# Kernel optimization log

Hardware: AMD Instinct MI355X
Metric: run time of the kernel (lower is better)

The kernel has to match this reference:

```python
import jax, jax.numpy as jnp
import numpy as np

HIDDEN = 1024
INTER = 4096
N_EXPERTS = 8


def geglu(x, w1, w2, w3):
    # x: [N, C], w1/w2: [C, I], w3: [I, C]
    return (jax.nn.gelu(x @ w1, approximate=False) * (x @ w2)) @ w3


def setup_inputs() -> dict:
    key = jax.random.key(0)
    ks = jax.random.split(key, 8)
    s = 0.02
    x = jax.random.normal(ks[0], (2, 2048, HIDDEN), dtype=jnp.float32)
    w1s = jax.random.normal(ks[1], (HIDDEN, INTER), dtype=jnp.float32) * s
    w2s = jax.random.normal(ks[2], (HIDDEN, INTER), dtype=jnp.float32) * s
    w3s = jax.random.normal(ks[3], (INTER, HIDDEN), dtype=jnp.float32) * s
    W1 = jax.random.normal(ks[4], (N_EXPERTS, HIDDEN, INTER), dtype=jnp.float32) * s
    W2 = jax.random.normal(ks[5], (N_EXPERTS, HIDDEN, INTER), dtype=jnp.float32) * s
    W3 = jax.random.normal(ks[6], (N_EXPERTS, INTER, HIDDEN), dtype=jnp.float32) * s
    Wg = jax.random.normal(ks[7], (HIDDEN, N_EXPERTS), dtype=jnp.float32) * s
    return {"x": x, "w1s": w1s, "w2s": w2s, "w3s": w3s,
            "W1": W1, "W2": W2, "W3": W3, "Wg": Wg}


def reference(x, w1s, w2s, w3s, W1, W2, W3, Wg):
    B, T, C = x.shape
    xf = x.reshape(-1, C)  # [N, C]
    shared = geglu(xf, w1s, w2s, w3s)  # [N, C]
    logits = xf @ Wg  # [N, E]
    # top-1 of softmax == argmax of logits (softmax is monotone);
    # NOTE: original torch code does NOT multiply by the routing prob.
    idx = jnp.argmax(logits, axis=-1)  # [N]
    final = jnp.zeros_like(xf)
    for e in range(N_EXPERTS):  # small fixed expert count
        y = geglu(xf, W1[e], W2[e], W3[e])  # [N, C]
        final = final + jnp.where((idx == e)[:, None], y, 0.0)
    return (shared + final).reshape(B, T, C)
```

## Files before the change

### kernel.cpp

```cpp
#include <hip/hip_runtime.h>
#include <stdint.h>

#define HIDDEN 1024
#define INTER  4096
#define NTOK   4096
#define HROWS  (2*NTOK)
#define MAXB1  40
#define MAXB2  72
#define NMAT   27

typedef unsigned short u16;
typedef unsigned int   u32;
typedef __bf16  bf16x8 __attribute__((ext_vector_type(8)));
typedef float   f32x4  __attribute__((ext_vector_type(4)));
typedef u32     u32x4  __attribute__((ext_vector_type(4)));

#define WAITVM(N) asm volatile("s_waitcnt vmcnt(" #N ")" ::: "memory")

__device__ __forceinline__ void hard_barrier() {
  asm volatile("" ::: "memory");
  __builtin_amdgcn_s_barrier();
  asm volatile("" ::: "memory");
}

__device__ __forceinline__ u16 f2bf(float f) {
  u32 u = __float_as_uint(f);
  u32 r = u + 0x7FFFu + ((u >> 16) & 1u);
  return (u16)(r >> 16);
}

__device__ __forceinline__ u32 cvt_pk_bf16(float lo, float hi) {
  u32 r;
  asm("v_cvt_pk_bf16_f32 %0, %1, %2" : "=v"(r) : "v"(lo), "v"(hi));
  return r;
}

__device__ __forceinline__ void glds16(const void* g, void* l) {
  __builtin_amdgcn_global_load_lds(
      (const __attribute__((address_space(1))) void*)g,
      (__attribute__((address_space(3))) void*)l, 16, 0, 0);
}


__global__ void k_init(int* cnt, int* fill) {
  if (threadIdx.x < 8) { cnt[threadIdx.x] = 0; fill[threadIdx.x] = 0; }
}

__global__ __launch_bounds__(256) void k_gate(const float* __restrict__ x,
                                              const float* __restrict__ wg,
                                              int* __restrict__ idx,
                                              int* __restrict__ cnt) {
  int wave = threadIdx.x >> 6, lane = threadIdx.x & 63;
  int t = blockIdx.x * 4 + wave;
  if (t >= NTOK) return;
  float acc[8];
  #pragma unroll
  for (int e = 0; e < 8; ++e) acc[e] = 0.f;
  const float* xr = x + (size_t)t * HIDDEN;
  for (int c = lane; c < HIDDEN; c += 64) {
    float xv = xr[c];
    const float* wrow = wg + (size_t)c * 8;
    #pragma unroll
    for (int e = 0; e < 8; ++e) acc[e] += xv * wrow[e];
  }
  #pragma unroll
  for (int e = 0; e < 8; ++e)
    for (int s = 32; s; s >>= 1) acc[e] += __shfl_xor(acc[e], s);
  if (lane == 0) {
    int best = 0; float bv = acc[0];
    #pragma unroll
    for (int e = 1; e < 8; ++e) if (acc[e] > bv) { bv = acc[e]; best = e; }
    idx[t] = best;
    atomicAdd(&cnt[best], 1);
  }
}

__global__ void k_cvt(const float* __restrict__ x, u16* __restrict__ xb, int n4) {
  int i = blockIdx.x * blockDim.x + threadIdx.x;
  if (i >= n4) return;
  float4 v = ((const float4*)x)[i];
  ushort4 o;
  o.x = f2bf(v.x); o.y = f2bf(v.y); o.z = f2bf(v.z); o.w = f2bf(v.w);
  ((ushort4*)xb)[i] = o;
}

__global__ void k_table(const int* __restrict__ cnt, int* __restrict__ off,
                        int4* __restrict__ tab1, int* __restrict__ nblk1,
                        int4* __restrict__ tab2, int* __restrict__ nblk2) {
  if (threadIdx.x != 0 || blockIdx.x != 0) return;
  int o = 0;
  int offs[8];
  for (int e = 0; e < 8; ++e) { offs[e] = o; off[e] = o; o += cnt[e]; }
  int nb = 0;
  for (int m = 0; m < NTOK / 256; ++m)
    tab1[nb++] = make_int4(8, m * 256, 256, 0);
  for (int e = 0; e < 8; ++e)
    for (int j = 0; j * 256 < cnt[e]; ++j) {
      int rows = cnt[e] - j * 256; if (rows > 256) rows = 256;
      tab1[nb++] = make_int4(e, NTOK + offs[e] + j * 256, rows, offs[e] + j * 256);
    }
  *nblk1 = nb;
  nb = 0;
  for (int m = 0; m < NTOK / 128; ++m)
    tab2[nb++] = make_int4(8, m * 128, 128, 0);
  for (int e = 0; e < 8; ++e)
    for (int j = 0; j * 128 < cnt[e]; ++j) {
      int rows = cnt[e] - j * 128; if (rows > 128) rows = 128;
      tab2[nb++] = make_int4(e, NTOK + offs[e] + j * 128, rows, offs[e] + j * 128);
    }
  *nblk2 = nb;
}

__global__ void k_scatter(const int* __restrict__ idx, const int* __restrict__ off,
                          int* __restrict__ fill, int* __restrict__ perm) {
  int t = blockIdx.x * blockDim.x + threadIdx.x;
  if (t >= NTOK) return;
  int e = idx[t];
  int p = atomicAdd(&fill[e], 1);
  perm[off[e] + p] = t;
}


__global__ __launch_bounds__(256) void k_wcvt(
    const float* __restrict__ w1s, const float* __restrict__ w2s,
    const float* __restrict__ w3s, const float* __restrict__ W1,
    const float* __restrict__ W2,  const float* __restrict__ W3,
    u16* __restrict__ Wb)
{
  int bid = blockIdx.x;
  int m = bid >> 9, pair = bid & 511;
  const float* src; int N, nkt, kt, pp2;
  if (m < 18) {
    N = INTER; nkt = 32;
    int mm = (m < 9) ? m : m - 9;
    const float* sp = (m < 9) ? w1s : w2s;
    const float* ep = (m < 9) ? W1 : W2;
    src = (mm == 0) ? sp : ep + (size_t)(mm - 1) * HIDDEN * INTER;
    kt = pair >> 4; pp2 = pair & 15;
  } else {
    N = HIDDEN; nkt = 128;
    int mm = m - 18;
    src = (mm == 0) ? w3s : W3 + (size_t)(mm - 1) * INTER * HIDDEN;
    kt = pair >> 2; pp2 = pair & 3;
  }

  __shared__ float tileF[32 * 256];
  int tid = threadIdx.x;
  const float* in0 = src + (size_t)(kt * 32) * N + pp2 * 256;
  #pragma unroll
  for (int i = 0; i < 8; ++i) {
    int f = tid + 256 * i;
    int k = f >> 6, c4 = f & 63;
    *(float4*)&tileF[k * 256 + c4 * 4] = *(const float4*)(in0 + (size_t)k * N + c4 * 4);
  }
  __syncthreads();

  int p2 = tid >> 7, n = tid & 127;
  int pidx = m * 1024 + (pp2 * 2 + p2) * nkt + kt;
  u16* outp = Wb + (size_t)pidx * 4096 + n * 32;
  #pragma unroll
  for (int s = 0; s < 4; ++s) {
    int k8 = s ^ ((n >> 1) & 3);
    const float* col = &tileF[(k8 * 8) * 256 + p2 * 128 + n];
    u32x4 pk;
    pk.x = cvt_pk_bf16(col[0],    col[256]);
    pk.y = cvt_pk_bf16(col[512],  col[768]);
    pk.z = cvt_pk_bf16(col[1024], col[1280]);
    pk.w = cvt_pk_bf16(col[1536], col[1792]);
    *(u32x4*)(outp + s * 8) = pk;
  }
}


#define MLP1_TILE(B, STG, WN)                                                        \
  do {                                                                               \
    const u16* LA = pAr  + (B) * 16384;                                              \
    const u16* L1 = pBr1 + (B) * 16384;                                              \
    const u16* L2 = pBr2 + (B) * 16384;                                              \
    bf16x8 af[8], f1[2], f2[2];                                                      \
    _Pragma("unroll")                                                                \
    for (int mi = 0; mi < 4; ++mi) af[mi] = *(const bf16x8*)(LA + mi * 512);         \
    _Pragma("unroll")                                                                \
    for (int ni = 0; ni < 2; ++ni) {                                                 \
      f1[ni] = *(const bf16x8*)(L1 + ni * 512);                                      \
      f2[ni] = *(const bf16x8*)(L2 + ni * 512);                                      \
    }                                                                                \
    if (STG) {                                                                       \
      char* Ld = smem + (((B) + 3) & 3) * 32768;                                     \
      glds16(srcA0, Ld + w * 2048);                                                  \
      glds16(srcA1, Ld + w * 2048 + 1024);                                           \
      srcA0 += 64; srcA1 += 64;                                                      \
    }                                                                                \
    __builtin_amdgcn_s_setprio(1);                                                   \
    _Pragma("unroll")                                                                \
    for (int mi = 0; mi < 4; ++mi) {                                                 \
      acc1[mi][0] = __builtin_amdgcn_mfma_f32_16x16x32_bf16(af[mi], f1[0], acc1[mi][0], 0, 0, 0); \
      acc1[mi][1] = __builtin_amdgcn_mfma_f32_16x16x32_bf16(af[mi], f1[1], acc1[mi][1], 0, 0, 0); \
      acc2[mi][0] = __builtin_amdgcn_mfma_f32_16x16x32_bf16(af[mi], f2[0], acc2[mi][0], 0, 0, 0); \
      acc2[mi][1] = __builtin_amdgcn_mfma_f32_16x16x32_bf16(af[mi], f2[1], acc2[mi][1], 0, 0, 0); \
    }                                                                                \
    __builtin_amdgcn_s_setprio(0);                                                   \
    hard_barrier();                                                                  \
    _Pragma("unroll")                                                                \
    for (int mi = 4; mi < 8; ++mi) af[mi] = *(const bf16x8*)(LA + mi * 512);         \
    if (STG) {                                                                       \
      char* Ld = smem + (((B) + 3) & 3) * 32768;                                     \
      glds16(srcB1, Ld + 16384 + w * 1024);                                          \
      glds16(srcB2, Ld + 24576 + w * 1024);                                          \
      srcB1 += 8192; srcB2 += 8192;                                                  \
    }                                                                                \
    __builtin_amdgcn_s_setprio(1);                                                   \
    _Pragma("unroll")                                                                \
    for (int mi = 4; mi < 8; ++mi) {                                                 \
      acc1[mi][0] = __builtin_amdgcn_mfma_f32_16x16x32_bf16(af[mi], f1[0], acc1[mi][0], 0, 0, 0); \
      acc1[mi][1] = __builtin_amdgcn_mfma_f32_16x16x32_bf16(af[mi], f1[1], acc1[mi][1], 0, 0, 0); \
      acc2[mi][0] = __builtin_amdgcn_mfma_f32_16x16x32_bf16(af[mi], f2[0], acc2[mi][0], 0, 0, 0); \
      acc2[mi][1] = __builtin_amdgcn_mfma_f32_16x16x32_bf16(af[mi], f2[1], acc2[mi][1], 0, 0, 0); \
    }                                                                                \
    __builtin_amdgcn_s_setprio(0);                                                   \
    WN;                                                                              \
    hard_barrier();                                                                  \
  } while (0)

__global__ __launch_bounds__(512, 2) void k_mlp1(
    const u16* __restrict__ xb, const u16* __restrict__ Wb,
    const int* __restrict__ perm, const int4* __restrict__ tab,
    const int* __restrict__ nblk, u16* __restrict__ Hbuf)
{
  int bx = blockIdx.x;
  if (bx >= *nblk) return;
  int4 te = tab[bx];
  int g = te.x, hrow0 = te.y, rows = te.z, pb = te.w;
  int m1 = (g == 8) ? 0 : 1 + g;
  int pp = blockIdx.y;
  int nbase = pp * 128;

  extern __shared__ __align__(16) char smem[];
  int tid = threadIdx.x;
  int w = tid >> 6, lane = tid & 63;
  int q = lane >> 4, rl = lane & 15;
  int mw = w >> 2, nw = w & 3;

  int tokj[2];
  #pragma unroll
  for (int j = 0; j < 2; ++j) {
    int r = w * 32 + j * 16 + (lane >> 2);
    int rc = (r < rows) ? r : (rows - 1);
    tokj[j] = (g == 8) ? (hrow0 + rc) : perm[pb + rc];
  }
  int gch = ((lane & 3) ^ ((lane >> 3) & 3)) * 16;

  const char* srcA0 = (const char*)xb + (size_t)tokj[0] * 2048 + gch;
  const char* srcA1 = (const char*)xb + (size_t)tokj[1] * 2048 + gch;
  const char* srcB1 = (const char*)Wb + ((size_t)m1 * 1024 + pp * 32) * 8192 + (tid << 4);
  const char* srcB2 = (const char*)Wb + ((size_t)(m1 + 9) * 1024 + pp * 32) * 8192 + (tid << 4);

  int co = (q ^ ((rl >> 1) & 3)) * 8;
  const u16* pAr  = (const u16*)smem + (mw * 128 + rl) * 32 + co;
  const u16* pBr1 = (const u16*)smem + 8192  + (nw * 32 + rl) * 32 + co;
  const u16* pBr2 = (const u16*)smem + 12288 + (nw * 32 + rl) * 32 + co;

  f32x4 acc1[8][2], acc2[8][2];
  f32x4 z = {0.f, 0.f, 0.f, 0.f};
  #pragma unroll
  for (int mi = 0; mi < 8; ++mi)
    #pragma unroll
    for (int ni = 0; ni < 2; ++ni) { acc1[mi][ni] = z; acc2[mi][ni] = z; }

  #pragma unroll
  for (int p = 0; p < 3; ++p) {
    char* Ld = smem + p * 32768;
    glds16(srcA0, Ld + w * 2048);
    glds16(srcA1, Ld + w * 2048 + 1024);
    srcA0 += 64; srcA1 += 64;
    glds16(srcB1, Ld + 16384 + w * 1024);
    glds16(srcB2, Ld + 24576 + w * 1024);
    srcB1 += 8192; srcB2 += 8192;
  }
  WAITVM(8);
  hard_barrier();

  for (int t0 = 0; t0 < 28; t0 += 4) {
    MLP1_TILE(0, 1, WAITVM(8));
    MLP1_TILE(1, 1, WAITVM(8));
    MLP1_TILE(2, 1, WAITVM(8));
    MLP1_TILE(3, 1, WAITVM(8));
  }
  MLP1_TILE(0, 1, WAITVM(8));
  MLP1_TILE(1, 0, WAITVM(4));
  MLP1_TILE(2, 0, WAITVM(0));
  MLP1_TILE(3, 0, (void)0);

  #pragma unroll
  for (int mi = 0; mi < 8; ++mi) {
    #pragma unroll
    for (int j = 0; j < 4; ++j) {
      int r = mw * 128 + mi * 16 + q * 4 + j;
      if (r < rows) {
        size_t hb = (size_t)(hrow0 + r) * INTER + nbase + nw * 32;
        #pragma unroll
        for (int ni = 0; ni < 2; ++ni) {
          float h1 = acc1[mi][ni][j];
          float h2 = acc2[mi][ni][j];
          float ge = 0.5f * h1 * (1.0f + erff(h1 * 0.7071067811865476f));
          Hbuf[hb + ni * 16 + rl] = f2bf(ge * h2);
        }
      }
    }
  }
}


#define MLP2_TILE(B, STG, WN)                                                        \
  do {                                                                               \
    const u16* LA = pAr + (B) * 12288;                                               \
    const u16* LB = pBr + (B) * 12288;                                               \
    bf16x8 af[4], bf[4];                                                             \
    _Pragma("unroll")                                                                \
    for (int mi = 0; mi < 4; ++mi) af[mi] = *(const bf16x8*)(LA + mi * 512);         \
    _Pragma("unroll")                                                                \
    for (int ni = 0; ni < 4; ++ni) bf[ni] = *(const bf16x8*)(LB + ni * 512);         \
    if (STG) {                                                                       \
      char* Ld = smem + (((B) + 3) & 3) * 24576;                                     \
      glds16(srcA0, Ld + w * 1024);              srcA0 += 64;                        \
      glds16(srcB0, Ld + 8192 + w * 1024);       srcB0 += 8192;                      \
      glds16(srcB1, Ld + 16384 + w * 1024);      srcB1 += 8192;                      \
    }                                                                                \
    __builtin_amdgcn_s_setprio(1);                                                   \
    _Pragma("unroll")                                                                \
    for (int mi = 0; mi < 4; ++mi)                                                   \
      _Pragma("unroll")                                                              \
      for (int ni = 0; ni < 4; ++ni)                                                 \
        acc[mi][ni] = __builtin_amdgcn_mfma_f32_16x16x32_bf16(af[mi], bf[ni], acc[mi][ni], 0, 0, 0); \
    __builtin_amdgcn_s_setprio(0);                                                   \
    WN;                                                                              \
    hard_barrier();                                                                  \
  } while (0)

__global__ __launch_bounds__(512, 2) void k_mlp2(
    const u16* __restrict__ Hbuf, const u16* __restrict__ Wb,
    const int* __restrict__ perm, const int4* __restrict__ tab,
    const int* __restrict__ nblk, float* __restrict__ out,
    float* __restrict__ yexp)
{
  int bx = blockIdx.x;
  if (bx >= *nblk) return;
  int4 te = tab[bx];
  int g = te.x, hrow0 = te.y, rows = te.z, pb = te.w;
  int m3 = (g == 8) ? 18 : 19 + g;
  int pp2 = blockIdx.y;

  extern __shared__ __align__(16) char smem[];
  int tid = threadIdx.x;
  int w = tid >> 6, lane = tid & 63;
  int q = lane >> 4, rl = lane & 15;
  int mw = w >> 2, nw = w & 3;

  int rr = w * 16 + (lane >> 2);
  int rc = (rr < rows) ? rr : (rows - 1);
  int hr = hrow0 + rc;
  int gch = ((lane & 3) ^ ((lane >> 3) & 3)) * 16;

  const char* srcA0 = (const char*)Hbuf + (size_t)hr * (INTER * 2) + gch;
  const char* srcB0 = (const char*)Wb + ((size_t)m3 * 1024 + (pp2 * 2) * 128) * 8192 + (tid << 4);
  const char* srcB1 = (const char*)Wb + ((size_t)m3 * 1024 + (pp2 * 2 + 1) * 128) * 8192 + (tid << 4);

  int co = (q ^ ((rl >> 1) & 3)) * 8;
  const u16* pAr = (const u16*)smem + (mw * 64 + rl) * 32 + co;
  const u16* pBr = (const u16*)smem + 4096 + (nw * 64 + rl) * 32 + co;

  f32x4 acc[4][4];
  f32x4 z = {0.f, 0.f, 0.f, 0.f};
  #pragma unroll
  for (int mi = 0; mi < 4; ++mi)
    #pragma unroll
    for (int ni = 0; ni < 4; ++ni) acc[mi][ni] = z;

  #pragma unroll
  for (int p = 0; p < 3; ++p) {
    char* Ld = smem + p * 24576;
    glds16(srcA0, Ld + w * 1024);          srcA0 += 64;
    glds16(srcB0, Ld + 8192 + w * 1024);   srcB0 += 8192;
    glds16(srcB1, Ld + 16384 + w * 1024);  srcB1 += 8192;
  }
  WAITVM(6);
  hard_barrier();

  for (int t0 = 0; t0 < 124; t0 += 4) {
    MLP2_TILE(0, 1, WAITVM(6));
    MLP2_TILE(1, 1, WAITVM(6));
    MLP2_TILE(2, 1, WAITVM(6));
    MLP2_TILE(3, 1, WAITVM(6));
  }
  MLP2_TILE(0, 1, WAITVM(6));
  MLP2_TILE(1, 0, WAITVM(3));
  MLP2_TILE(2, 0, WAITVM(0));
  MLP2_TILE(3, 0, (void)0);

  float* dstb = (g == 8) ? out : yexp;
  #pragma unroll
  for (int mi = 0; mi < 4; ++mi) {
    #pragma unroll
    for (int j = 0; j < 4; ++j) {
      int r = mw * 64 + mi * 16 + q * 4 + j;
      if (r < rows) {
        int tok = (g == 8) ? (hrow0 + r) : perm[pb + r];
        size_t ob = (size_t)tok * HIDDEN + pp2 * 256 + nw * 64;
        #pragma unroll
        for (int ni = 0; ni < 4; ++ni)
          dstb[ob + ni * 16 + rl] = acc[mi][ni][j];
      }
    }
  }
}

__global__ void k_add(float* __restrict__ out, const float* __restrict__ yexp, int n4) {
  int i = blockIdx.x * blockDim.x + threadIdx.x;
  if (i >= n4) return;
  float4 a = ((const float4*)out)[i];
  float4 b = ((const float4*)yexp)[i];
  a.x += b.x; a.y += b.y; a.z += b.z; a.w += b.w;
  ((float4*)out)[i] = a;
}


extern "C" void kernel_launch(void* const* d_in, const int* in_sizes, int n_in,
                              void* d_out, int out_size, void* d_ws, size_t ws_size,
                              hipStream_t stream) {
  const float* x   = (const float*)d_in[0];
  const float* w1s = (const float*)d_in[1];
  const float* w2s = (const float*)d_in[2];
  const float* w3s = (const float*)d_in[3];
  const float* W1  = (const float*)d_in[4];
  const float* W2  = (const float*)d_in[5];
  const float* W3  = (const float*)d_in[6];
  const float* Wg  = (const float*)d_in[7];
  float* out = (float*)d_out;

  char* ws = (char*)d_ws;
  size_t o_xb   = 0;
  size_t o_H    = o_xb   + (size_t)NTOK * HIDDEN * 2;
  size_t o_yexp = o_H    + (size_t)HROWS * INTER * 2;
  size_t o_Wb   = o_yexp + (size_t)NTOK * HIDDEN * 4;
  size_t o_idx  = o_Wb   + (size_t)NMAT * 1024 * 8192;
  size_t o_perm = o_idx  + (size_t)NTOK * 4;
  size_t o_cnt  = o_perm + (size_t)NTOK * 4;
  size_t o_off  = o_cnt  + 32;
  size_t o_fill = o_off  + 32;
  size_t o_nb1  = o_fill + 32;
  size_t o_nb2  = o_nb1  + 32;
  size_t o_tab1 = o_nb2  + 32;
  size_t o_tab2 = o_tab1 + (size_t)MAXB1 * 16;
  size_t need   = o_tab2 + (size_t)MAXB2 * 16;
  if (ws_size < need) return;

  u16*  xb   = (u16*)(ws + o_xb);
  u16*  Hbuf = (u16*)(ws + o_H);
  float* yexp = (float*)(ws + o_yexp);
  u16*  Wb   = (u16*)(ws + o_Wb);
  int*  idx  = (int*)(ws + o_idx);
  int*  perm = (int*)(ws + o_perm);
  int*  cnt  = (int*)(ws + o_cnt);
  int*  off  = (int*)(ws + o_off);
  int*  fill = (int*)(ws + o_fill);
  int*  nblk1 = (int*)(ws + o_nb1);
  int*  nblk2 = (int*)(ws + o_nb2);
  int4* tab1 = (int4*)(ws + o_tab1);
  int4* tab2 = (int4*)(ws + o_tab2);

  k_init<<<1, 64, 0, stream>>>(cnt, fill);
  k_gate<<<NTOK / 4, 256, 0, stream>>>(x, Wg, idx, cnt);
  k_cvt<<<(NTOK * HIDDEN / 4) / 256, 256, 0, stream>>>(x, xb, NTOK * HIDDEN / 4);
  k_wcvt<<<NMAT * 512, 256, 0, stream>>>(w1s, w2s, w3s, W1, W2, W3, Wb);
  k_table<<<1, 1, 0, stream>>>(cnt, off, tab1, nblk1, tab2, nblk2);
  k_scatter<<<NTOK / 256, 256, 0, stream>>>(idx, off, fill, perm);
  k_mlp1<<<dim3(MAXB1, INTER / 128), 512, 131072, stream>>>(xb, Wb, perm, tab1, nblk1, Hbuf);
  k_mlp2<<<dim3(MAXB2, HIDDEN / 256), 512, 98304, stream>>>(Hbuf, Wb, perm, tab2, nblk2, out, yexp);
  k_add<<<(NTOK * HIDDEN / 4) / 256, 256, 0, stream>>>(out, yexp, NTOK * HIDDEN / 4);
}
```

Baseline: 524.0 us.

## Fuse x bf16 conversion into gate, retune MLP1 pipeline and MLP2 tiling

New measurement: 549.4 us. 1.05x slower.

```diff
diff --git a/kernel.cpp b/kernel.cpp
--- a/kernel.cpp
+++ b/kernel.cpp
@@ -49,7 +49,8 @@
 __global__ __launch_bounds__(256) void k_gate(const float* __restrict__ x,
                                               const float* __restrict__ wg,
                                               int* __restrict__ idx,
-                                              int* __restrict__ cnt) {
+                                              int* __restrict__ cnt,
+                                              u16* __restrict__ xb) {
   int wave = threadIdx.x >> 6, lane = threadIdx.x & 63;
   int t = blockIdx.x * 4 + wave;
   if (t >= NTOK) return;
@@ -57,8 +58,10 @@
   #pragma unroll
   for (int e = 0; e < 8; ++e) acc[e] = 0.f;
   const float* xr = x + (size_t)t * HIDDEN;
+  u16* xbr = xb + (size_t)t * HIDDEN;
   for (int c = lane; c < HIDDEN; c += 64) {
     float xv = xr[c];
+    xbr[c] = f2bf(xv);
     const float* wrow = wg + (size_t)c * 8;
     #pragma unroll
     for (int e = 0; e < 8; ++e) acc[e] += xv * wrow[e];
@@ -73,15 +76,6 @@
     idx[t] = best;
     atomicAdd(&cnt[best], 1);
   }
-}
-
-__global__ void k_cvt(const float* __restrict__ x, u16* __restrict__ xb, int n4) {
-  int i = blockIdx.x * blockDim.x + threadIdx.x;
-  if (i >= n4) return;
-  float4 v = ((const float4*)x)[i];
-  ushort4 o;
-  o.x = f2bf(v.x); o.y = f2bf(v.y); o.z = f2bf(v.z); o.w = f2bf(v.w);
-  ((ushort4*)xb)[i] = o;
 }
 
 __global__ void k_table(const int* __restrict__ cnt, int* __restrict__ off,
@@ -172,50 +166,55 @@
 }
 
 
-#define MLP1_TILE(B, STG, WN)                                                        \
+#define M1P(B, STG, WN)                                                              \
   do {                                                                               \
     const u16* LA = pAr  + (B) * 16384;                                              \
     const u16* L1 = pBr1 + (B) * 16384;                                              \
     const u16* L2 = pBr2 + (B) * 16384;                                              \
-    bf16x8 af[8], f1[2], f2[2];                                                      \
-    _Pragma("unroll")                                                                \
-    for (int mi = 0; mi < 4; ++mi) af[mi] = *(const bf16x8*)(LA + mi * 512);         \
-    _Pragma("unroll")                                                                \
-    for (int ni = 0; ni < 2; ++ni) {                                                 \
-      f1[ni] = *(const bf16x8*)(L1 + ni * 512);                                      \
-      f2[ni] = *(const bf16x8*)(L2 + ni * 512);                                      \
-    }                                                                                \
+    char* Ld = smem + (((B) + 2) & 3) * 32768;                                       \
+    bf16x8 af[8], b1[2], b2[2];                                                      \
+            \
+    af[0] = *(const bf16x8*)(LA);                                                    \
+    af[1] = *(const bf16x8*)(LA + 512);                                              \
+    af[2] = *(const bf16x8*)(LA + 1024);                                             \
+    af[3] = *(const bf16x8*)(LA + 1536);                                             \
+    b1[0] = *(const bf16x8*)(L1);                                                    \
+    b1[1] = *(const bf16x8*)(L1 + 512);                                              \
+    b2[0] = *(const bf16x8*)(L2);                                                    \
+    b2[1] = *(const bf16x8*)(L2 + 512);                                              \
     if (STG) {                                                                       \
-      char* Ld = smem + (((B) + 3) & 3) * 32768;                                     \
       glds16(srcA0, Ld + w * 2048);                                                  \
       glds16(srcA1, Ld + w * 2048 + 1024);                                           \
       srcA0 += 64; srcA1 += 64;                                                      \
     }                                                                                \
+    hard_barrier();                                                                  \
     __builtin_amdgcn_s_setprio(1);                                                   \
     _Pragma("unroll")                                                                \
     for (int mi = 0; mi < 4; ++mi) {                                                 \
-      acc1[mi][0] = __builtin_amdgcn_mfma_f32_16x16x32_bf16(af[mi], f1[0], acc1[mi][0], 0, 0, 0); \
-      acc1[mi][1] = __builtin_amdgcn_mfma_f32_16x16x32_bf16(af[mi], f1[1], acc1[mi][1], 0, 0, 0); \
-      acc2[mi][0] = __builtin_amdgcn_mfma_f32_16x16x32_bf16(af[mi], f2[0], acc2[mi][0], 0, 0, 0); \
-      acc2[mi][1] = __builtin_amdgcn_mfma_f32_16x16x32_bf16(af[mi], f2[1], acc2[mi][1], 0, 0, 0); \
+      acc1[mi][0] = __builtin_amdgcn_mfma_f32_16x16x32_bf16(af[mi], b1[0], acc1[mi][0], 0, 0, 0); \
+      acc1[mi][1] = __builtin_amdgcn_mfma_f32_16x16x32_bf16(af[mi], b1[1], acc1[mi][1], 0, 0, 0); \
+      acc2[mi][0] = __builtin_amdgcn_mfma_f32_16x16x32_bf16(af[mi], b2[0], acc2[mi][0], 0, 0, 0); \
+      acc2[mi][1] = __builtin_amdgcn_mfma_f32_16x16x32_bf16(af[mi], b2[1], acc2[mi][1], 0, 0, 0); \
     }                                                                                \
     __builtin_amdgcn_s_setprio(0);                                                   \
     hard_barrier();                                                                  \
-    _Pragma("unroll")                                                                \
-    for (int mi = 4; mi < 8; ++mi) af[mi] = *(const bf16x8*)(LA + mi * 512);         \
+    \
+    af[4] = *(const bf16x8*)(LA + 2048);                                             \
+    af[5] = *(const bf16x8*)(LA + 2560);                                             \
+    af[6] = *(const bf16x8*)(LA + 3072);                                             \
+    af[7] = *(const bf16x8*)(LA + 3584);                                             \
     if (STG) {                                                                       \
-      char* Ld = smem + (((B) + 3) & 3) * 32768;                                     \
-      glds16(srcB1, Ld + 16384 + w * 1024);                                          \
-      glds16(srcB2, Ld + 24576 + w * 1024);                                          \
-      srcB1 += 8192; srcB2 += 8192;                                                  \
+      glds16(srcB1, Ld + 16384 + w * 1024);  srcB1 += 8192;                          \
+      glds16(srcB2, Ld + 24576 + w * 1024);  srcB2 += 8192;                          \
     }                                                                                \
+    hard_barrier();                                                                  \
     __builtin_amdgcn_s_setprio(1);                                                   \
     _Pragma("unroll")                                                                \
     for (int mi = 4; mi < 8; ++mi) {                                                 \
-      acc1[mi][0] = __builtin_amdgcn_mfma_f32_16x16x32_bf16(af[mi], f1[0], acc1[mi][0], 0, 0, 0); \
-      acc1[mi][1] = __builtin_amdgcn_mfma_f32_16x16x32_bf16(af[mi], f1[1], acc1[mi][1], 0, 0, 0); \
-      acc2[mi][0] = __builtin_amdgcn_mfma_f32_16x16x32_bf16(af[mi], f2[0], acc2[mi][0], 0, 0, 0); \
-      acc2[mi][1] = __builtin_amdgcn_mfma_f32_16x16x32_bf16(af[mi], f2[1], acc2[mi][1], 0, 0, 0); \
+      acc1[mi][0] = __builtin_amdgcn_mfma_f32_16x16x32_bf16(af[mi], b1[0], acc1[mi][0], 0, 0, 0); \
+      acc1[mi][1] = __builtin_amdgcn_mfma_f32_16x16x32_bf16(af[mi], b1[1], acc1[mi][1], 0, 0, 0); \
+      acc2[mi][0] = __builtin_amdgcn_mfma_f32_16x16x32_bf16(af[mi], b2[0], acc2[mi][0], 0, 0, 0); \
+      acc2[mi][1] = __builtin_amdgcn_mfma_f32_16x16x32_bf16(af[mi], b2[1], acc2[mi][1], 0, 0, 0); \
     }                                                                                \
     __builtin_amdgcn_s_setprio(0);                                                   \
     WN;                                                                              \
@@ -252,8 +251,8 @@
 
   const char* srcA0 = (const char*)xb + (size_t)tokj[0] * 2048 + gch;
   const char* srcA1 = (const char*)xb + (size_t)tokj[1] * 2048 + gch;
-  const char* srcB1 = (const char*)Wb + ((size_t)m1 * 1024 + pp * 32) * 8192 + (tid << 4);
-  const char* srcB2 = (const char*)Wb + ((size_t)(m1 + 9) * 1024 + pp * 32) * 8192 + (tid << 4);
+  const char* srcB1 = (const char*)Wb + ((size_t)m1 * 1024 + pp * 32) * 8192 + w * 1024 + (lane << 4);
+  const char* srcB2 = (const char*)Wb + ((size_t)(m1 + 9) * 1024 + pp * 32) * 8192 + w * 1024 + (lane << 4);
 
   int co = (q ^ ((rl >> 1) & 3)) * 8;
   const u16* pAr  = (const u16*)smem + (mw * 128 + rl) * 32 + co;
@@ -268,28 +267,27 @@
     for (int ni = 0; ni < 2; ++ni) { acc1[mi][ni] = z; acc2[mi][ni] = z; }
 
   #pragma unroll
-  for (int p = 0; p < 3; ++p) {
+  for (int p = 0; p < 2; ++p) {
     char* Ld = smem + p * 32768;
     glds16(srcA0, Ld + w * 2048);
     glds16(srcA1, Ld + w * 2048 + 1024);
     srcA0 += 64; srcA1 += 64;
-    glds16(srcB1, Ld + 16384 + w * 1024);
-    glds16(srcB2, Ld + 24576 + w * 1024);
-    srcB1 += 8192; srcB2 += 8192;
-  }
-  WAITVM(8);
+    glds16(srcB1, Ld + 16384 + w * 1024);  srcB1 += 8192;
+    glds16(srcB2, Ld + 24576 + w * 1024);  srcB2 += 8192;
+  }
+  WAITVM(4);
   hard_barrier();
 
-  for (int t0 = 0; t0 < 28; t0 += 4) {
-    MLP1_TILE(0, 1, WAITVM(8));
-    MLP1_TILE(1, 1, WAITVM(8));
-    MLP1_TILE(2, 1, WAITVM(8));
-    MLP1_TILE(3, 1, WAITVM(8));
-  }
-  MLP1_TILE(0, 1, WAITVM(8));
-  MLP1_TILE(1, 0, WAITVM(4));
-  MLP1_TILE(2, 0, WAITVM(0));
-  MLP1_TILE(3, 0, (void)0);
+  for (int r = 0; r < 7; ++r) {
+    M1P(0, 1, WAITVM(4));
+    M1P(1, 1, WAITVM(4));
+    M1P(2, 1, WAITVM(4));
+    M1P(3, 1, WAITVM(4));
+  }
+  M1P(0, 1, WAITVM(4));
+  M1P(1, 1, WAITVM(4));
+  M1P(2, 0, WAITVM(0));
+  M1P(3, 0, (void)0);
 
   #pragma unroll
   for (int mi = 0; mi < 8; ++mi) {
@@ -311,21 +309,23 @@
 }
 
 
-#define MLP2_TILE(B, STG, WN)                                                        \
+#define M2_TILE(B, STG, WN)                                                          \
   do {                                                                               \
-    const u16* LA = pAr + (B) * 12288;                                               \
-    const u16* LB = pBr + (B) * 12288;                                               \
+    const u16* LA = pAr + (B) * 8192;                                                \
+    const u16* LB = pBr + (B) * 8192;                                                \
+    if (STG) {                                                                       \
+      char* Ld = smem + (((B) + 2) % 3) * 16384;                                     \
+      glds16(srcA0, Ld + w * 2048);                                                  \
+      glds16(srcA1, Ld + w * 2048 + 1024);                                           \
+      glds16(srcB0, Ld + 8192 + w * 2048);                                           \
+      glds16(srcB0 + 1024, Ld + 8192 + w * 2048 + 1024);                             \
+      srcA0 += 64; srcA1 += 64; srcB0 += 8192;                                       \
+    }                                                                                \
     bf16x8 af[4], bf[4];                                                             \
     _Pragma("unroll")                                                                \
     for (int mi = 0; mi < 4; ++mi) af[mi] = *(const bf16x8*)(LA + mi * 512);         \
     _Pragma("unroll")                                                                \
     for (int ni = 0; ni < 4; ++ni) bf[ni] = *(const bf16x8*)(LB + ni * 512);         \
-    if (STG) {                                                                       \
-      char* Ld = smem + (((B) + 3) & 3) * 24576;                                     \
-      glds16(srcA0, Ld + w * 1024);              srcA0 += 64;                        \
-      glds16(srcB0, Ld + 8192 + w * 1024);       srcB0 += 8192;                      \
-      glds16(srcB1, Ld + 16384 + w * 1024);      srcB1 += 8192;                      \
-    }                                                                                \
     __builtin_amdgcn_s_setprio(1);                                                   \
     _Pragma("unroll")                                                                \
     for (int mi = 0; mi < 4; ++mi)                                                   \
@@ -337,7 +337,7 @@
     hard_barrier();                                                                  \
   } while (0)
 
-__global__ __launch_bounds__(512, 2) void k_mlp2(
+__global__ __launch_bounds__(256, 3) void k_mlp2(
     const u16* __restrict__ Hbuf, const u16* __restrict__ Wb,
     const int* __restrict__ perm, const int4* __restrict__ tab,
     const int* __restrict__ nblk, float* __restrict__ out,
@@ -348,22 +348,27 @@
   int4 te = tab[bx];
   int g = te.x, hrow0 = te.y, rows = te.z, pb = te.w;
   int m3 = (g == 8) ? 18 : 19 + g;
-  int pp2 = blockIdx.y;
+  int pp = blockIdx.y;
+  int nbase = pp * 128;
 
   extern __shared__ __align__(16) char smem[];
   int tid = threadIdx.x;
   int w = tid >> 6, lane = tid & 63;
   int q = lane >> 4, rl = lane & 15;
-  int mw = w >> 2, nw = w & 3;
-
-  int rr = w * 16 + (lane >> 2);
-  int rc = (rr < rows) ? rr : (rows - 1);
-  int hr = hrow0 + rc;
+  int mw = w >> 1, nw = w & 1;
+
+  int hr[2];
+  #pragma unroll
+  for (int j = 0; j < 2; ++j) {
+    int r = w * 32 + j * 16 + (lane >> 2);
+    int rc = (r < rows) ? r : (rows - 1);
+    hr[j] = hrow0 + rc;
+  }
   int gch = ((lane & 3) ^ ((lane >> 3) & 3)) * 16;
 
-  const char* srcA0 = (const char*)Hbuf + (size_t)hr * (INTER * 2) + gch;
-  const char* srcB0 = (const char*)Wb + ((size_t)m3 * 1024 + (pp2 * 2) * 128) * 8192 + (tid << 4);
-  const char* srcB1 = (const char*)Wb + ((size_t)m3 * 1024 + (pp2 * 2 + 1) * 128) * 8192 + (tid << 4);
+  const char* srcA0 = (const char*)Hbuf + (size_t)hr[0] * (INTER * 2) + gch;
+  const char* srcA1 = (const char*)Hbuf + (size_t)hr[1] * (INTER * 2) + gch;
+  const char* srcB0 = (const char*)Wb + ((size_t)m3 * 1024 + pp * 128) * 8192 + w * 2048 + (lane << 4);
 
   int co = (q ^ ((rl >> 1) & 3)) * 8;
   const u16* pAr = (const u16*)smem + (mw * 64 + rl) * 32 + co;
@@ -377,25 +382,24 @@
     for (int ni = 0; ni < 4; ++ni) acc[mi][ni] = z;
 
   #pragma unroll
-  for (int p = 0; p < 3; ++p) {
-    char* Ld = smem + p * 24576;
-    glds16(srcA0, Ld + w * 1024);          srcA0 += 64;
-    glds16(srcB0, Ld + 8192 + w * 1024);   srcB0 += 8192;
-    glds16(srcB1, Ld + 16384 + w * 1024);  srcB1 += 8192;
-  }
-  WAITVM(6);
+  for (int p = 0; p < 2; ++p) {
+    char* Ld = smem + p * 16384;
+    glds16(srcA0, Ld + w * 2048);
+    glds16(srcA1, Ld + w * 2048 + 1024);
+    glds16(srcB0, Ld + 8192 + w * 2048);
+    glds16(srcB0 + 1024, Ld + 8192 + w * 2048 + 1024);
+    srcA0 += 64; srcA1 += 64; srcB0 += 8192;
+  }
+  WAITVM(4);
   hard_barrier();
 
-  for (int t0 = 0; t0 < 124; t0 += 4) {
-    MLP2_TILE(0, 1, WAITVM(6));
-    MLP2_TILE(1, 1, WAITVM(6));
-    MLP2_TILE(2, 1, WAITVM(6));
-    MLP2_TILE(3, 1, WAITVM(6));
-  }
-  MLP2_TILE(0, 1, WAITVM(6));
-  MLP2_TILE(1, 0, WAITVM(3));
-  MLP2_TILE(2, 0, WAITVM(0));
-  MLP2_TILE(3, 0, (void)0);
+  for (int r = 0; r < 42; ++r) {
+    M2_TILE(0, 1, WAITVM(4));
+    M2_TILE(1, 1, WAITVM(4));
+    M2_TILE(2, 1, WAITVM(4));
+  }
+  M2_TILE(0, 0, WAITVM(0));
+  M2_TILE(1, 0, (void)0);
 
   float* dstb = (g == 8) ? out : yexp;
   #pragma unroll
@@ -405,7 +409,7 @@
       int r = mw * 64 + mi * 16 + q * 4 + j;
       if (r < rows) {
         int tok = (g == 8) ? (hrow0 + r) : perm[pb + r];
-        size_t ob = (size_t)tok * HIDDEN + pp2 * 256 + nw * 64;
+        size_t ob = (size_t)tok * HIDDEN + nbase + nw * 64;
         #pragma unroll
         for (int ni = 0; ni < 4; ++ni)
           dstb[ob + ni * 16 + rl] = acc[mi][ni][j];
@@ -469,12 +473,11 @@
   int4* tab2 = (int4*)(ws + o_tab2);
 
   k_init<<<1, 64, 0, stream>>>(cnt, fill);
-  k_gate<<<NTOK / 4, 256, 0, stream>>>(x, Wg, idx, cnt);
-  k_cvt<<<(NTOK * HIDDEN / 4) / 256, 256, 0, stream>>>(x, xb, NTOK * HIDDEN / 4);
+  k_gate<<<NTOK / 4, 256, 0, stream>>>(x, Wg, idx, cnt, xb);
   k_wcvt<<<NMAT * 512, 256, 0, stream>>>(w1s, w2s, w3s, W1, W2, W3, Wb);
   k_table<<<1, 1, 0, stream>>>(cnt, off, tab1, nblk1, tab2, nblk2);
   k_scatter<<<NTOK / 256, 256, 0, stream>>>(idx, off, fill, perm);
   k_mlp1<<<dim3(MAXB1, INTER / 128), 512, 131072, stream>>>(xb, Wb, perm, tab1, nblk1, Hbuf);
-  k_mlp2<<<dim3(MAXB2, HIDDEN / 256), 512, 98304, stream>>>(Hbuf, Wb, perm, tab2, nblk2, out, yexp);
+  k_mlp2<<<dim3(MAXB2, HIDDEN / 128), 256, 49152, stream>>>(Hbuf, Wb, perm, tab2, nblk2, out, yexp);
   k_add<<<(NTOK * HIDDEN / 4) / 256, 256, 0, stream>>>(out, yexp, NTOK * HIDDEN / 4);
 }
```
